# Kernel tuning notes

Hardware: AMD Instinct MI355X
Metric: run time of the kernel (lower is better)

The kernel has to match this reference:

```python
import jax, jax.numpy as jnp
import numpy as np
from jax.scipy.linalg import expm

B, D, CUT, LAYERS = 256, 4, 10, 4
K = D * (D - 1) // 2            # beamsplitter pairs per interferometer
P = 4 * K + 6 * D               # params per CVQNN layer (=48 for D=4)


def _ops(c):
    a = jnp.diag(jnp.sqrt(jnp.arange(1, c, dtype=jnp.float32)), k=1).astype(jnp.complex64)
    return a, a.T, jnp.arange(c, dtype=jnp.float32)


def _apply_single(state, U, m):
    t = jnp.tensordot(state, U, axes=((m + 1,), (1,)))
    return jnp.moveaxis(t, -1, m + 1)


def _apply_two(state, U4, i, j):
    t = jnp.tensordot(state, U4, axes=((i + 1, j + 1), (2, 3)))
    return jnp.moveaxis(t, (-2, -1), (i + 1, j + 1))


def _mul_diag(state, diag, m, d, c):
    return state * diag.reshape((1,) * (m + 1) + (c,) + (1,) * (d - m - 1))


def _interferometer(state, th, ph, vph, a, adag, n, d, c):
    pairs = [(i, j) for i in range(d) for j in range(i + 1, d)]
    Aab = jnp.kron(adag, a)  # adag_i a_j on a mode pair

    def gen(t, p):
        tc = t.astype(jnp.complex64)
        pc = p.astype(jnp.complex64)
        return tc * (jnp.exp(1j * pc) * Aab - jnp.exp(-1j * pc) * Aab.conj().T)

    U = jax.vmap(expm)(jax.vmap(gen)(th, ph)).reshape(len(pairs), c, c, c, c)
    for k, (i, j) in enumerate(pairs):
        state = _apply_two(state, U[k], i, j)
    nc = n.astype(jnp.complex64)
    for m in range(d):
        state = _mul_diag(state, jnp.exp(1j * vph[m].astype(jnp.complex64) * nc), m, d, c)
    return state


def _layer(state, w, a, adag, n, d, c):
    k = d * (d - 1) // 2
    o = 0
    th1 = w[o:o + k]; o += k
    ph1 = w[o:o + k]; o += k
    vp1 = w[o:o + d]; o += d
    rsq = w[o:o + d]; o += d
    th2 = w[o:o + k]; o += k
    ph2 = w[o:o + k]; o += k
    vp2 = w[o:o + d]; o += d
    rd = w[o:o + d]; o += d
    phd = w[o:o + d]; o += d
    kap = w[o:o + d]

    state = _interferometer(state, th1, ph1, vp1, a, adag, n, d, c)
    # per-mode squeezing S(r) = exp(r/2 (a^2 - adag^2))
    Ss = jax.vmap(lambda r: expm(0.5 * r.astype(jnp.complex64) * (a @ a - adag @ adag)))(rsq)
    for m in range(d):
        state = _apply_single(state, Ss[m], m)
    state = _interferometer(state, th2, ph2, vp2, a, adag, n, d, c)
    # per-mode displacement D(alpha)
    alpha = rd.astype(jnp.complex64) * jnp.exp(1j * phd.astype(jnp.complex64))
    Ds = jax.vmap(lambda al: expm(al * adag - jnp.conj(al) * a))(alpha)
    for m in range(d):
        state = _apply_single(state, Ds[m], m)
    # per-mode Kerr: diag(exp(i kappa n^2))
    nc = n.astype(jnp.complex64)
    for m in range(d):
        state = _mul_diag(state, jnp.exp(1j * kap[m].astype(jnp.complex64) * nc * nc), m, d, c)
    return state


def _forward(inputs, weights):
    d, c = D, CUT
    a, adag, n = _ops(c)
    # BatchPrepare: per mode |psi> = Displacement(r, 0) Squeezing(0.5, pi/2) |0>
    z = 0.5j  # r=0.5, phi=pi/2
    S0 = expm(0.5 * (jnp.conj(z) * (a @ a) - z * (adag @ adag)))
    psi0 = S0[:, 0]  # S |0>
    Dm = jax.vmap(lambda r: expm(r.astype(jnp.complex64) * (adag - a)))(inputs.reshape(-1))
    psi = (Dm @ psi0).reshape(inputs.shape[0], d, c)  # [B, d, c]
    # tensor product over modes -> [B, c, ..., c]
    state = psi[:, 0]
    for m in range(1, d):
        state = jnp.einsum('b...,bc->b...c', state, psi[:, m])
    for l in range(LAYERS):
        state = _layer(state, weights[l], a, adag, n, d, c)
    probs = jnp.abs(state) ** 2  # no normalization (Config(normalize=False))
    outs = [jnp.sum(_mul_diag(probs, n, m, d, c), axis=tuple(range(1, d + 1))) for m in range(d)]
    return jnp.stack(outs, axis=1)  # [B, modes] mean photon numbers


def setup_inputs() -> dict:
    key = jax.random.key(0)
    k1, k2 = jax.random.split(key)
    inputs = 0.3 * jax.random.normal(k1, (B, D), dtype=jnp.float32)
    cvqnn_weights = 0.1 * jax.random.normal(k2, (LAYERS, P), dtype=jnp.float32)
    return {"inputs": inputs, "cvqnn_weights": cvqnn_weights, "batch_size": B}


def reference(inputs, cvqnn_weights, batch_size):
    assert inputs.shape[0] == batch_size
    return _forward(inputs, cvqnn_weights)
```

## Files before the change

### kernel.cpp

```cpp
#include <hip/hip_runtime.h>
#include <hip/hip_bf16.h>

#define CUT 10
#define NB 256
#define NLAYERS 4
#define WSTRIDE 48

#define R_DM 0
#define R_SQ 1024
#define R_DS 1040
#define R_BS 1056
#define NRSLOTS 1968

#define F0 1110
#define F1 111
#define F2 11
#define F3 1
#define ST_PHYS 11100

#define LUT_A  0
#define LUT_B  60
#define LUT_C  120
#define LUT_I  234
#define LUT_S  253
#define LUT_IS 259
#define LUT_K  260
#define LUT_N  300

typedef __hip_bfloat16 bf16;

__device__ __forceinline__ float readv(const void* p, int i, int isf32) {
  if (isf32) return ((const float*)p)[i];
  return __bfloat162float(((const bf16*)p)[i]);
}

__device__ __forceinline__ void rmacL(float2& a, float2 mm, float2 v) {
  asm("v_pk_fma_f32 %0, %1, %2, %0 op_sel:[0,0,0] op_sel_hi:[0,1,1]"
      : "+v"(a) : "v"(mm), "v"(v));
}
__device__ __forceinline__ void rmacH(float2& a, float2 mm, float2 v) {
  asm("v_pk_fma_f32 %0, %1, %2, %0 op_sel:[1,0,0] op_sel_hi:[1,1,1]"
      : "+v"(a) : "v"(mm), "v"(v));
}

__device__ __forceinline__ float2 cmul(float2 u, float2 v) {
  float2 d;
  asm("v_pk_mul_f32 %0, %1, %2 op_sel:[0,0] op_sel_hi:[0,1]\n\t"
      "v_pk_fma_f32 %0, %1, %2, %0 op_sel:[1,1,0] op_sel_hi:[1,0,1] neg_lo:[1,0,0]"
      : "=&v"(d) : "v"(u), "v"(v));
  return d;
}

__device__ __forceinline__ float2 loF(const float4& q) { return make_float2(q.x, q.y); }
__device__ __forceinline__ float2 hiF(const float4& q) { return make_float2(q.z, q.w); }

__device__ const signed char g_perm[16][3] = {
  {18,-1,-1},{19,-1,-1},{16, 0,-1},{17, 1,-1},{20,36,-1},{21,37,-1},
  {14, 6,34},{15, 7,35},{22,30,-1},{23,31,-1},{12, 8, 4},{13, 9, 5},
  {24,28,32},{25,29,33},{10,26, 2},{11,27, 3}
};

__global__ void sniff_dtype(const void* p, int n_elems, int* flag) {
  __shared__ float red[256];
  const unsigned short* h = (const unsigned short*)p;
  int t = threadIdx.x;
  float mx = 0.f;
  for (int i = t; i < n_elems; i += 256) {
    unsigned short u = h[i];
    bf16 bv = *(const bf16*)&u;
    float v = fabsf(__bfloat162float(bv));
    if (!(v < 1e30f)) v = 1e30f;
    mx = fmaxf(mx, v);
  }
  red[t] = mx;
  __syncthreads();
  for (int off = 128; off > 0; off >>= 1) {
    if (t < off) red[t] = fmaxf(red[t], red[t + off]);
    __syncthreads();
  }
  if (t == 0) *flag = (red[0] > 1000.f) ? 1 : 0;
}

__global__ void build_gens(float* rslots, float2* s0, const void* inp,
                           const void* w, const int* flag) {
  int s = blockIdx.x;
  int t = threadIdx.x;
  if (t >= 100) return;
// ... 149 lines not shown
    if (t < 100) R[t] = acc;
    __syncthreads();
  }
  if (t < 100) G[t] = R[t];
}

__device__ __forceinline__ void gate_fs(const void* w, int isf32, int l, int half,
                                        int g, float& f0, float& f1, float& f3,
                                        float& fdc) {
  int po = l*WSTRIDE + (half ? 26 : 6);
  int vo = l*WSTRIDE + (half ? 32 : 12);
  f0 = 0.f; f1 = 0.f; f3 = 0.f;
  switch (g) {
    case 0: fdc = readv(w, po+0, isf32) - readv(w, po+1, isf32); break;
    case 1: fdc = readv(w, po+1, isf32) - readv(w, po+2, isf32); break;
    case 2: f0 = -readv(w, po+3, isf32); fdc = readv(w, po+2, isf32); break;
    case 3: fdc = readv(w, po+3, isf32) - readv(w, po+4, isf32); break;
    case 4: f1 = -readv(w, po+5, isf32); fdc = readv(w, po+4, isf32); break;
    default: {
      float vp0 = readv(w, vo+0, isf32), vp1 = readv(w, vo+1, isf32);
      float vp2 = readv(w, vo+2, isf32), vp3 = readv(w, vo+3, isf32);
      if (half) {
        vp0 -= readv(w, l*WSTRIDE+40+0, isf32);
        vp1 -= readv(w, l*WSTRIDE+40+1, isf32);
        vp2 -= readv(w, l*WSTRIDE+40+2, isf32);
        vp3 -= readv(w, l*WSTRIDE+40+3, isf32);
      }
      f0 = vp0; f1 = vp1; f3 = vp3;
      fdc = vp2 + readv(w, po+5, isf32) - vp3;
    }
  }
}

#define LOADQ(DST, P) do { _Pragma("unroll") \
  for (int q_ = 0; q_ < 5; ++q_) DST[q_] = Uq[(P)*5 + q_]; } while (0)

#define BS_PAIR(UA, R0)                                                        \
  {                                                                            \
    float2 a0 = make_float2(0.f,0.f), a1 = make_float2(0.f,0.f);               \
    _Pragma("unroll")                                                          \
    for (int j = 0; j < 5; ++j) if (2*j < sd) {                                \
      const float2 m0 = (j==0)?loF(UA[0]):(j==1)?hiF(UA[0]):(j==2)?loF(UA[1])  \
                        :(j==3)?hiF(UA[1]):loF(UA[2]);                         \
      const float2 m1 = (j==0)?hiF(UA[2]):(j==1)?loF(UA[3]):(j==2)?hiF(UA[3])  \
                        :(j==3)?loF(UA[4]):hiF(UA[4]);                         \
      rmacL(a0, m0, v[2*j]); rmacH(a0, m0, v[2*j+1]);                          \
      rmacL(a1, m1, v[2*j]); rmacH(a1, m1, v[2*j+1]);                          \
    }                                                                          \
    a0 = cmul(a0, rot); rot = cmul(rot, step);                                 \
    base[(R0)*se] = a0;                                                        \
    if ((R0) + 1 < sd) {                                                       \
      a1 = cmul(a1, rot); rot = cmul(rot, step);                               \
      base[((R0)+1)*se] = a1;                                                  \
    }                                                                          \
  }

template<int sI, int sJ, int sA, int sB, bool INROT>
__device__ __forceinline__ void bs_chunk(
    float2* st, const float* __restrict__ U, int sd,
    int hi10, int lo10, int lo, int N,
    float2 rot, float2 step, float2 ir, float2 istep)
{
  constexpr int se = sI - sJ;
  float2* base = st + hi10*sA + lo10*sB + lo*sI + (N - lo)*sJ;
  float2 v[10];
#pragma unroll
  for (int k = 0; k < 10; ++k) {
    if (k < sd) {
      float2 tv = base[k*se];
      if (INROT) { tv = cmul(tv, ir); ir = cmul(ir, istep); }
      v[k] = tv;
    } else {
      v[k] = make_float2(0.f, 0.f);
    }
  }
  const float4* Uq = (const float4*)U;
  float4 ua[5], ub[5];
  LOADQ(ua, 0);
#pragma unroll
  for (int p = 0; p < 5; p += 2) {
    if (2*p < sd) {
      if (2*p + 2 < sd) LOADQ(ub, p + 1);
      BS_PAIR(ua, 2*p);
    }
    if (2*p + 2 < sd) {
      if (2*p + 4 < sd) LOADQ(ua, p + 2);
      BS_PAIR(ub, 2*p + 2);
    }
  }
}

template<int sI, int sJ, int sA, int sB, bool INROT>
__device__ __forceinline__ void bs_gate(
    float2* st, const float* __restrict__ Ub, const float2* __restrict__ lut,
    int g, int lane, int ch0, int ch1, int ch2)
{
  const float2 step  = lut[LUT_S + g];
  const float2 istep = INROT ? lut[LUT_IS] : make_float2(1.f, 0.f);
#pragma unroll
  for (int r = 0; r < 3; ++r) {
    const int c = (r == 0) ? ch0 : (r == 1) ? ch1 : ch2;
    if (c >= 0) {
      int N = c >> 1;
      int spec = ((c & 1) << 6) + lane;
      if (spec < 100) {
        int lo = max(0, N - 9);
        const int sd = __builtin_amdgcn_readfirstlane(min(9, N) - lo + 1);
        int hi10 = spec / 10, lo10 = spec % 10;
        float2 rot = cmul(cmul(lut[LUT_A + g*10 + hi10], lut[LUT_B + g*10 + lo10]),
                          lut[LUT_C + g*19 + N]);
        float2 ir = INROT ? lut[LUT_I + N] : make_float2(1.f, 0.f);
        bs_chunk<sI,sJ,sA,sB,INROT>(st, Ub + N*100, sd, hi10, lo10, lo, N,
                                    rot, step, ir, istep);
      }
    }
  }
}

#define SM_PAIR(UA, R0)                                                        \
  {                                                                            \
    float2 a0 = make_float2(0.f,0.f), a1 = make_float2(0.f,0.f);               \
    _Pragma("unroll")                                                          \
    for (int j = 0; j < 5; ++j) {                                              \
      const float2 m0 = (j==0)?loF(UA[0]):(j==1)?hiF(UA[0]):(j==2)?loF(UA[1])  \
                        :(j==3)?hiF(UA[1]):loF(UA[2]);                         \
      const float2 m1 = (j==0)?hiF(UA[2]):(j==1)?loF(UA[3]):(j==2)?hiF(UA[3])  \
                        :(j==3)?loF(UA[4]):hiF(UA[4]);                         \
      rmacL(a0, m0, v[2*j]); rmacH(a0, m0, v[2*j+1]);                          \
      rmacL(a1, m1, v[2*j]); rmacH(a1, m1, v[2*j+1]);                          \
    }                                                                          \
    if (KERR) {                                                                \
      a0 = cmul(a0, cmul(kb, lut[LUT_K + 30 + (R0)]));                         \
      a1 = cmul(a1, cmul(kb, lut[LUT_K + 30 + (R0) + 1]));                     \
    }                                                                          \
    base[(R0)*sM] = a0;                                                        \
    base[((R0)+1)*sM] = a1;                                                    \
  }

template<int sM, int pA, int pB, int pC, bool KERR>
__device__ __forceinline__ void sm_gate(
    float2* st, const float* __restrict__ U, const float2* __restrict__ lut,
    bool smv, int q0, int q1, int q2)
{
  if (!smv) return;
  float2* base = st + q0*pA + q1*pB + q2*pC;
  float2 kb = make_float2(1.f, 0.f);
  if (KERR) kb = cmul(cmul(lut[LUT_K + q0], lut[LUT_K + 10 + q1]),
                      lut[LUT_K + 20 + q2]);
  float2 v[10];
#pragma unroll
  for (int k = 0; k < 10; ++k) v[k] = base[k*sM];
  const float4* Uq = (const float4*)U;
  float4 ua[5], ub[5];
  LOADQ(ua, 0);
#pragma unroll
  for (int p = 0; p < 5; p += 2) {
    {
      if (p < 4) LOADQ(ub, p + 1);
      SM_PAIR(ua, 2*p);
    }
    if (p + 1 < 5) {
      if (p + 2 < 5) LOADQ(ua, p + 2);
      SM_PAIR(ub, 2*(p + 1));
    }
  }
}

__global__ __launch_bounds__(1024, 4)
void fused_circuit(
    const float* __restrict__ rslots, const float2* __restrict__ s0,
    const void* __restrict__ w, const int* __restrict__ flag,
    float* __restrict__ out)
{
  __shared__ float2 st[ST_PHYS];
  __shared__ __align__(16) float smU[3200];
  __shared__ __align__(16) float bsU[2*1900];
  __shared__ float2 lut[LUT_N];
  __shared__ float2 psi[4][10];
  __shared__ float redw[64];
  const int b = blockIdx.x, t = threadIdx.x;
  const int wv = t >> 6, lane = t & 63;
  const int isf32 = *flag;

  const int ch0 = g_perm[wv][0], ch1 = g_perm[wv][1], ch2 = g_perm[wv][2];
  const bool smv = (t < 1000);
  const int q0 = t / 100, q1 = (t / 10) % 10, q2 = t % 10;

  if (t < 40) {
    int m = t / 10, r = t % 10;
    const float* Dmr = rslots + (size_t)(R_DM + b*4 + m) * 100;
    float2 acc = make_float2(0.f, 0.f);
    for (int c = 0; c < 10; ++c) {
      float a = Dmr[r*10 + c];
      float2 vv = s0[c * 10];
      acc.x += a * vv.x;
      acc.y += a * vv.y;
    }
    psi[m][r] = acc;
  }
  for (int i = t; i < 800; i += 1024)
    ((float4*)smU)[i] = ((const float4*)(rslots + (size_t)R_SQ * 100))[i];
  for (int i = t; i < 475; i += 1024)
    ((float4*)bsU)[i] = ((const float4*)(rslots + (size_t)R_BS * 100))[i];
  __syncthreads();
  for (int e = t; e < 10000; e += 1024) {
    int ph = e + e/10 + e/100;
    float2 z  = psi[0][e/1000];
    float2 w1 = psi[1][(e/100)%10];
    float2 r1 = make_float2(z.x*w1.x - z.y*w1.y, z.x*w1.y + z.y*w1.x);
    float2 w2 = psi[2][(e/10)%10];
    float2 r2 = make_float2(r1.x*w2.x - r1.y*w2.y, r1.x*w2.y + r1.y*w2.x);
    float2 w3 = psi[3][e%10];
    st[ph] = make_float2(r2.x*w3.x - r2.y*w3.y, r2.x*w3.y + r2.y*w3.x);
  }
  __syncthreads();

  float4 pf;
  auto pf_load = [&](int next) {
    if (next < 48 && t < 475)
      pf = ((const float4*)(rslots + (size_t)(R_BS + next*19) * 100))[t];
  };
  auto pf_store = [&](int next) {
    if (next < 48 && t < 475)
      ((float4*)(bsU + (next & 1) * 1900))[t] = pf;
  };

#pragma unroll 1
  for (int l = 0; l < NLAYERS; ++l) {
#pragma unroll 1
    for (int half = 0; half < 2; ++half) {
      const int g6 = l*12 + half*6;

      {
        const int po = l*WSTRIDE + (half ? 26 : 6);
        if (t < LUT_N) {
          float ang = 0.f;
          if (t < 120) {
            int isB = (t >= 60);
            int id = isB ? t - 60 : t;
            int g = id / 10, q = id % 10;
            float f0, f1, f3, fd;
            gate_fs(w, isf32, l, half, g, f0, f1, f3, fd);
            ang = (isB ? f1 : f0) * (float)q;
          } else if (t < 234) {
            int id = t - 120; int g = id / 19, N = id % 19;
            float f0, f1, f3, fd;
            gate_fs(w, isf32, l, half, g, f0, f1, f3, fd);
            int lo = max(0, N - 9);
            ang = f3 * (float)N + fd * (float)lo;
          } else if (t < 253) {
            int N = t - 234; int lo = max(0, N - 9);
            ang = -readv(w, po + 0, isf32) * (float)lo;
          } else if (t < 259) {
            int g = t - 253;
            float f0, f1, f3, fd;
            gate_fs(w, isf32, l, half, g, f0, f1, f3, fd);
            ang = fd;
          } else if (t == 259) {
            ang = -readv(w, po + 0, isf32);
          } else {
            int id = t - 260; int m = id / 10, q = id % 10;
            if (half) {
              float kap = readv(w, l*WSTRIDE + 44 + m, isf32);
              float pd  = readv(w, l*WSTRIDE + 40 + m, isf32);
              ang = kap * (float)(q*q) + pd * (float)q;
            }
          }
          float sn, cs; sincosf(ang, &sn, &cs);
          lut[t] = make_float2(cs, sn);
        }
        __syncthreads();
      }

      pf_load(g6+1);
      bs_gate<F0,F1,F2,F3,true >(st, bsU+((g6+0)&1)*1900, lut, 0, lane, ch0,ch1,ch2);
      pf_store(g6+1);
      __syncthreads();
      pf_load(g6+2);
      bs_gate<F0,F2,F1,F3,false>(st, bsU+((g6+1)&1)*1900, lut, 1, lane, ch0,ch1,ch2);
      pf_store(g6+2);
      __syncthreads();
      pf_load(g6+3);
      bs_gate<F0,F3,F1,F2,false>(st, bsU+((g6+2)&1)*1900, lut, 2, lane, ch0,ch1,ch2);
      pf_store(g6+3);
      __syncthreads();
      pf_load(g6+4);
      bs_gate<F1,F2,F0,F3,false>(st, bsU+((g6+3)&1)*1900, lut, 3, lane, ch0,ch1,ch2);
      pf_store(g6+4);
      __syncthreads();
      pf_load(g6+5);
      bs_gate<F1,F3,F0,F2,false>(st, bsU+((g6+4)&1)*1900, lut, 4, lane, ch0,ch1,ch2);
      pf_store(g6+5);
      __syncthreads();
      pf_load(g6+6);
      bs_gate<F2,F3,F0,F1,false>(st, bsU+((g6+5)&1)*1900, lut, 5, lane, ch0,ch1,ch2);
      pf_store(g6+6);
      __syncthreads();

      const int ub_ = (half == 0) ? (l*4) : (16 + l*4);
      sm_gate<F0,F1,F2,F3,false>(st, smU+(ub_+0)*100, lut, smv, q0,q1,q2);
      __syncthreads();
      sm_gate<F1,F0,F2,F3,false>(st, smU+(ub_+1)*100, lut, smv, q0,q1,q2);
      __syncthreads();
      sm_gate<F2,F0,F1,F3,false>(st, smU+(ub_+2)*100, lut, smv, q0,q1,q2);
      __syncthreads();
      if (half)
        sm_gate<F3,F0,F1,F2,true >(st, smU+(ub_+3)*100, lut, smv, q0,q1,q2);
      else
        sm_gate<F3,F0,F1,F2,false>(st, smU+(ub_+3)*100, lut, smv, q0,q1,q2);
      __syncthreads();
    }
  }

  float a0 = 0.f, a1 = 0.f, a2 = 0.f, a3 = 0.f;
  for (int e = t; e < 10000; e += 1024) {
    int ph = e + e/10 + e/100;
    float2 z = st[ph];
    float pz = z.x*z.x + z.y*z.y;
    a0 += pz * (float)(e/1000);
    a1 += pz * (float)((e/100)%10);
    a2 += pz * (float)((e/10)%10);
    a3 += pz * (float)(e%10);
  }
  for (int off2 = 32; off2 > 0; off2 >>= 1) {
    a0 += __shfl_down(a0, off2, 64);
    a1 += __shfl_down(a1, off2, 64);
    a2 += __shfl_down(a2, off2, 64);
    a3 += __shfl_down(a3, off2, 64);
  }
  if (lane == 0) {
    redw[wv*4+0] = a0; redw[wv*4+1] = a1;
    redw[wv*4+2] = a2; redw[wv*4+3] = a3;
  }
  __syncthreads();
  if (t < 4) {
    float s = 0.f;
    for (int ww = 0; ww < 16; ++ww) s += redw[ww*4 + t];
    out[b*4 + t] = s;
  }
}

extern "C" void kernel_launch(void* const* d_in, const int* in_sizes, int n_in,
                              void* d_out, int out_size, void* d_ws, size_t ws_size,
// ... 15 lines not shown
```

Before: 349.4 us.

## Double-buffer phase LUT and interleave beamsplitter chunk loads across chunks

The per-half phase LUT is now double-buffered and built for the next half during the last squeezing gate, which removes one barrier and the serialized LUT-build phase per half. The beamsplitter gate is restructured so two chunks' state vectors are loaded up front and the third chunk's load overlaps the previous chunk's compute. Rotation recurrences now use doubled steps, giving two independent chains. The per-wave channel indices are made scalar with readfirstlane. This raises register pressure because two 10-element vectors are live at once.

After: 424.6 us. +21.5%, slower.

```diff
diff --git a/kernel.cpp b/kernel.cpp
--- a/kernel.cpp
+++ b/kernel.cpp
@@ -25,7 +25,10 @@
 #define LUT_S  253
 #define LUT_IS 259
 #define LUT_K  260
-#define LUT_N  300
+#define LUT_S2 300
+#define LUT_IS2 306
+#define LUT_N  307
+#define LUT_PAD 320
 
 typedef __hip_bfloat16 bf16;
 
@@ -50,9 +53,6 @@
       : "=&v"(d) : "v"(u), "v"(v));
   return d;
 }
-
-__device__ __forceinline__ float2 loF(const float4& q) { return make_float2(q.x, q.y); }
-__device__ __forceinline__ float2 hiF(const float4& q) { return make_float2(q.z, q.w); }
 
 __device__ const signed char g_perm[16][3] = {
   {18,-1,-1},{19,-1,-1},{16, 0,-1},{17, 1,-1},{20,36,-1},{21,37,-1},
@@ -268,138 +268,209 @@
   }
 }
 
-#define LOADQ(DST, P) do { _Pragma("unroll") \
-  for (int q_ = 0; q_ < 5; ++q_) DST[q_] = Uq[(P)*5 + q_]; } while (0)
-
-#define BS_PAIR(UA, R0)                                                        \
-  {                                                                            \
-    float2 a0 = make_float2(0.f,0.f), a1 = make_float2(0.f,0.f);               \
-    _Pragma("unroll")                                                          \
-    for (int j = 0; j < 5; ++j) if (2*j < sd) {                                \
-      const float2 m0 = (j==0)?loF(UA[0]):(j==1)?hiF(UA[0]):(j==2)?loF(UA[1])  \
-                        :(j==3)?hiF(UA[1]):loF(UA[2]);                         \
-      const float2 m1 = (j==0)?hiF(UA[2]):(j==1)?loF(UA[3]):(j==2)?hiF(UA[3])  \
-                        :(j==3)?loF(UA[4]):hiF(UA[4]);                         \
-      rmacL(a0, m0, v[2*j]); rmacH(a0, m0, v[2*j+1]);                          \
-      rmacL(a1, m1, v[2*j]); rmacH(a1, m1, v[2*j+1]);                          \
-    }                                                                          \
-    a0 = cmul(a0, rot); rot = cmul(rot, step);                                 \
-    base[(R0)*se] = a0;                                                        \
-    if ((R0) + 1 < sd) {                                                       \
-      a1 = cmul(a1, rot); rot = cmul(rot, step);                               \
-      base[((R0)+1)*se] = a1;                                                  \
-    }                                                                          \
+__device__ __forceinline__ void build_lut(float2* lb, const void* w, int isf32,
+                                          int l, int half, int t) {
+  const int po = l*WSTRIDE + (half ? 26 : 6);
+  if (t < LUT_N) {
+    float ang = 0.f;
+    if (t < 120) {
+      int isB = (t >= 60);
+      int id = isB ? t - 60 : t;
+      int g = id / 10, q = id % 10;
+      float f0, f1, f3, fd;
+      gate_fs(w, isf32, l, half, g, f0, f1, f3, fd);
+      ang = (isB ? f1 : f0) * (float)q;
+    } else if (t < 234) {
+      int id = t - 120; int g = id / 19, N = id % 19;
+      float f0, f1, f3, fd;
+      gate_fs(w, isf32, l, half, g, f0, f1, f3, fd);
+      int lo = max(0, N - 9);
+      ang = f3 * (float)N + fd * (float)lo;
+    } else if (t < 253) {
+      int N = t - 234; int lo = max(0, N - 9);
+      ang = -readv(w, po + 0, isf32) * (float)lo;
+    } else if (t < 259) {
+      int g = t - 253;
+      float f0, f1, f3, fd;
+      gate_fs(w, isf32, l, half, g, f0, f1, f3, fd);
+      ang = fd;
+    } else if (t == 259) {
+      ang = -readv(w, po + 0, isf32);
+    } else if (t < 300) {
+      int id = t - 260; int m = id / 10, q = id % 10;
+      if (half) {
+        float kap = readv(w, l*WSTRIDE + 44 + m, isf32);
+        float pd  = readv(w, l*WSTRIDE + 40 + m, isf32);
+        ang = kap * (float)(q*q) + pd * (float)q;
+      }
+    } else if (t < 306) {
+      int g = t - 300;
+      float f0, f1, f3, fd;
+      gate_fs(w, isf32, l, half, g, f0, f1, f3, fd);
+      ang = 2.f * fd;
+    } else {
+      ang = -2.f * readv(w, po + 0, isf32);
+    }
+    float sn, cs; sincosf(ang, &sn, &cs);
+    lb[t] = make_float2(cs, sn);
+  }
+}
+
+#define BS_SETUP(IDX, C)                                                     \
+  int N##IDX = 0, sd##IDX = 0, hiA##IDX = 0, loA##IDX = 0;                   \
+  bool ok##IDX = false; float2* b##IDX = st;                                 \
+  if ((C) >= 0) {                                                            \
+    N##IDX = (C) >> 1;                                                       \
+    int spec_ = (((C) & 1) << 6) + lane;                                     \
+    int lo_ = max(0, N##IDX - 9);                                            \
+    sd##IDX = __builtin_amdgcn_readfirstlane(min(9, N##IDX) - lo_ + 1);      \
+    ok##IDX = (spec_ < 100);                                                 \
+    int spc_ = ok##IDX ? spec_ : 0;                                          \
+    hiA##IDX = spc_ / 10; loA##IDX = spc_ % 10;                              \
+    b##IDX = st + hiA##IDX*sA + loA##IDX*sB + lo_*sI + (N##IDX - lo_)*sJ;    \
+  }
+
+#define BS_LOAD(VV, IDX)                                                     \
+  { _Pragma("unroll")                                                        \
+    for (int k = 0; k < 10; ++k)                                             \
+      VV[k] = (k < sd##IDX) ? b##IDX[k*se] : make_float2(0.f, 0.f); }
+
+#define BS_INROT(VV, IDX)                                                    \
+  if (INROT && sd##IDX > 0) {                                                \
+    float2 ir0 = L[LUT_I + N##IDX];                                          \
+    float2 ir1 = cmul(ir0, istep1);                                          \
+    _Pragma("unroll")                                                        \
+    for (int k = 0; k < 10; k += 2) {                                        \
+      VV[k]   = cmul(VV[k],   ir0); ir0 = cmul(ir0, istep2);                 \
+      VV[k+1] = cmul(VV[k+1], ir1); ir1 = cmul(ir1, istep2);                 \
+    }                                                                        \
+  }
+
+#define BS_ROWPAIR(R0, VV)                                                   \
+  {                                                                          \
+    float2 a0 = make_float2(0.f,0.f), a1 = make_float2(0.f,0.f);             \
+    _Pragma("unroll")                                                        \
+    for (int j = 0; j < 5; ++j) if (2*j < sd_) {                             \
+      const float2 m0 = (j==0)?make_float2(qa0.x,qa0.y)                      \
+                       :(j==1)?make_float2(qa0.z,qa0.w)                      \
+                       :(j==2)?make_float2(qa1.x,qa1.y)                      \
+                       :(j==3)?make_float2(qa1.z,qa1.w)                      \
+                       :make_float2(qa2.x,qa2.y);                            \
+      const float2 m1 = (j==0)?make_float2(qa2.z,qa2.w)                      \
+                       :(j==1)?make_float2(qa3.x,qa3.y)                      \
+                       :(j==2)?make_float2(qa3.z,qa3.w)                      \
+                       :(j==3)?make_float2(qa4.x,qa4.y)                      \
+                       :make_float2(qa4.z,qa4.w);                            \
+      rmacL(a0, m0, VV[2*j]); rmacH(a0, m0, VV[2*j+1]);                      \
+      rmacL(a1, m1, VV[2*j]); rmacH(a1, m1, VV[2*j+1]);                      \
+    }                                                                        \
+    a0 = cmul(a0, rot0);                                                     \
+    if (ok_) bb[(R0)*se] = a0;                                               \
+    if ((R0) + 1 < sd_) {                                                    \
+      a1 = cmul(a1, rot1);                                                   \
+      if (ok_) bb[((R0)+1)*se] = a1;                                         \
+    }                                                                        \
+    rot0 = cmul(rot0, step2); rot1 = cmul(rot1, step2);                      \
+  }
+
+#define BS_COMP(VV, IDX)                                                     \
+  if (sd##IDX > 0) {                                                         \
+    const int sd_ = sd##IDX; const bool ok_ = ok##IDX;                       \
+    float2* bb = b##IDX;                                                     \
+    const float4* Uq = (const float4*)(Ub + N##IDX*100);                     \
+    float2 rot0 = cmul(cmul(L[LUT_A + g*10 + hiA##IDX],                      \
+                            L[LUT_B + g*10 + loA##IDX]),                     \
+                       L[LUT_C + g*19 + N##IDX]);                            \
+    float2 rot1 = cmul(rot0, step1);                                         \
+    float4 qa0,qa1,qa2,qa3,qa4;                                              \
+    qa0=Uq[0]; qa1=Uq[1]; qa2=Uq[2]; qa3=Uq[3]; qa4=Uq[4];                   \
+    BS_ROWPAIR(0, VV)                                                        \
+    if (sd_ > 2) { qa0=Uq[5]; qa1=Uq[6]; qa2=Uq[7]; qa3=Uq[8]; qa4=Uq[9];    \
+      BS_ROWPAIR(2, VV) }                                                    \
+    if (sd_ > 4) { qa0=Uq[10];qa1=Uq[11];qa2=Uq[12];qa3=Uq[13];qa4=Uq[14];   \
+      BS_ROWPAIR(4, VV) }                                                    \
+    if (sd_ > 6) { qa0=Uq[15];qa1=Uq[16];qa2=Uq[17];qa3=Uq[18];qa4=Uq[19];   \
+      BS_ROWPAIR(6, VV) }                                                    \
+    if (sd_ > 8) { qa0=Uq[20];qa1=Uq[21];qa2=Uq[22];qa3=Uq[23];qa4=Uq[24];   \
+      BS_ROWPAIR(8, VV) }                                                    \
   }
 
 template<int sI, int sJ, int sA, int sB, bool INROT>
-__device__ __forceinline__ void bs_chunk(
-    float2* st, const float* __restrict__ U, int sd,
-    int hi10, int lo10, int lo, int N,
-    float2 rot, float2 step, float2 ir, float2 istep)
+__device__ __forceinline__ void bs_gate(
+    float2* st, const float* __restrict__ Ub, const float2* __restrict__ L,
+    int g, int lane, int ch0, int ch1, int ch2)
 {
   constexpr int se = sI - sJ;
-  float2* base = st + hi10*sA + lo10*sB + lo*sI + (N - lo)*sJ;
-  float2 v[10];
-#pragma unroll
-  for (int k = 0; k < 10; ++k) {
-    if (k < sd) {
-      float2 tv = base[k*se];
-      if (INROT) { tv = cmul(tv, ir); ir = cmul(ir, istep); }
-      v[k] = tv;
-    } else {
-      v[k] = make_float2(0.f, 0.f);
-    }
-  }
-  const float4* Uq = (const float4*)U;
-  float4 ua[5], ub[5];
-  LOADQ(ua, 0);
-#pragma unroll
-  for (int p = 0; p < 5; p += 2) {
-    if (2*p < sd) {
-      if (2*p + 2 < sd) LOADQ(ub, p + 1);
-      BS_PAIR(ua, 2*p);
-    }
-    if (2*p + 2 < sd) {
-      if (2*p + 4 < sd) LOADQ(ua, p + 2);
-      BS_PAIR(ub, 2*p + 2);
-    }
-  }
-}
-
-template<int sI, int sJ, int sA, int sB, bool INROT>
-__device__ __forceinline__ void bs_gate(
-    float2* st, const float* __restrict__ Ub, const float2* __restrict__ lut,
-    int g, int lane, int ch0, int ch1, int ch2)
-{
-  const float2 step  = lut[LUT_S + g];
-  const float2 istep = INROT ? lut[LUT_IS] : make_float2(1.f, 0.f);
-#pragma unroll
-  for (int r = 0; r < 3; ++r) {
-    const int c = (r == 0) ? ch0 : (r == 1) ? ch1 : ch2;
-    if (c >= 0) {
-      int N = c >> 1;
-      int spec = ((c & 1) << 6) + lane;
-      if (spec < 100) {
-        int lo = max(0, N - 9);
-        const int sd = __builtin_amdgcn_readfirstlane(min(9, N) - lo + 1);
-        int hi10 = spec / 10, lo10 = spec % 10;
-        float2 rot = cmul(cmul(lut[LUT_A + g*10 + hi10], lut[LUT_B + g*10 + lo10]),
-                          lut[LUT_C + g*19 + N]);
-        float2 ir = INROT ? lut[LUT_I + N] : make_float2(1.f, 0.f);
-        bs_chunk<sI,sJ,sA,sB,INROT>(st, Ub + N*100, sd, hi10, lo10, lo, N,
-                                    rot, step, ir, istep);
-      }
-    }
-  }
-}
-
-#define SM_PAIR(UA, R0)                                                        \
-  {                                                                            \
-    float2 a0 = make_float2(0.f,0.f), a1 = make_float2(0.f,0.f);               \
-    _Pragma("unroll")                                                          \
-    for (int j = 0; j < 5; ++j) {                                              \
-      const float2 m0 = (j==0)?loF(UA[0]):(j==1)?hiF(UA[0]):(j==2)?loF(UA[1])  \
-                        :(j==3)?hiF(UA[1]):loF(UA[2]);                         \
-      const float2 m1 = (j==0)?hiF(UA[2]):(j==1)?loF(UA[3]):(j==2)?hiF(UA[3])  \
-                        :(j==3)?loF(UA[4]):hiF(UA[4]);                         \
-      rmacL(a0, m0, v[2*j]); rmacH(a0, m0, v[2*j+1]);                          \
-      rmacL(a1, m1, v[2*j]); rmacH(a1, m1, v[2*j+1]);                          \
-    }                                                                          \
-    if (KERR) {                                                                \
-      a0 = cmul(a0, cmul(kb, lut[LUT_K + 30 + (R0)]));                         \
-      a1 = cmul(a1, cmul(kb, lut[LUT_K + 30 + (R0) + 1]));                     \
-    }                                                                          \
-    base[(R0)*sM] = a0;                                                        \
-    base[((R0)+1)*sM] = a1;                                                    \
+  const float2 step1  = L[LUT_S + g];
+  const float2 step2  = L[LUT_S2 + g];
+  const float2 istep1 = L[LUT_IS];
+  const float2 istep2 = L[LUT_IS2];
+
+  float2 vA[10], vB[10];
+  BS_SETUP(0, ch0)
+  BS_SETUP(1, ch1)
+  BS_SETUP(2, ch2)
+  BS_LOAD(vA, 0)
+  BS_LOAD(vB, 1)
+  BS_INROT(vA, 0)
+  BS_COMP(vA, 0)
+  BS_LOAD(vA, 2)
+  BS_INROT(vB, 1)
+  BS_COMP(vB, 1)
+  BS_INROT(vA, 2)
+  BS_COMP(vA, 2)
+}
+
+#define SM_PAIR(R0)                                                          \
+  {                                                                          \
+    float2 a0 = make_float2(0.f,0.f), a1 = make_float2(0.f,0.f);             \
+    _Pragma("unroll")                                                        \
+    for (int j = 0; j < 5; ++j) {                                            \
+      const float2 m0 = (j==0)?make_float2(qa0.x,qa0.y)                      \
+                       :(j==1)?make_float2(qa0.z,qa0.w)                      \
+                       :(j==2)?make_float2(qa1.x,qa1.y)                      \
+                       :(j==3)?make_float2(qa1.z,qa1.w)                      \
+                       :make_float2(qa2.x,qa2.y);                            \
+      const float2 m1 = (j==0)?make_float2(qa2.z,qa2.w)                      \
+                       :(j==1)?make_float2(qa3.x,qa3.y)                      \
+                       :(j==2)?make_float2(qa3.z,qa3.w)                      \
+                       :(j==3)?make_float2(qa4.x,qa4.y)                      \
+                       :make_float2(qa4.z,qa4.w);                            \
+      rmacL(a0, m0, v[2*j]); rmacH(a0, m0, v[2*j+1]);                        \
+      rmacL(a1, m1, v[2*j]); rmacH(a1, m1, v[2*j+1]);                        \
+    }                                                                        \
+    if (KERR) {                                                              \
+      a0 = cmul(a0, cmul(kb, L[LUT_K + 30 + (R0)]));                         \
+      a1 = cmul(a1, cmul(kb, L[LUT_K + 30 + (R0) + 1]));                     \
+    }                                                                        \
+    base[(R0)*sM]   = a0;                                                    \
+    base[((R0)+1)*sM] = a1;                                                  \
   }
 
 template<int sM, int pA, int pB, int pC, bool KERR>
 __device__ __forceinline__ void sm_gate(
-    float2* st, const float* __restrict__ U, const float2* __restrict__ lut,
+    float2* st, const float* __restrict__ U, const float2* __restrict__ L,
     bool smv, int q0, int q1, int q2)
 {
   if (!smv) return;
   float2* base = st + q0*pA + q1*pB + q2*pC;
   float2 kb = make_float2(1.f, 0.f);
-  if (KERR) kb = cmul(cmul(lut[LUT_K + q0], lut[LUT_K + 10 + q1]),
-                      lut[LUT_K + 20 + q2]);
+  if (KERR) kb = cmul(cmul(L[LUT_K + q0], L[LUT_K + 10 + q1]), L[LUT_K + 20 + q2]);
   float2 v[10];
 #pragma unroll
   for (int k = 0; k < 10; ++k) v[k] = base[k*sM];
   const float4* Uq = (const float4*)U;
-  float4 ua[5], ub[5];
-  LOADQ(ua, 0);
-#pragma unroll
-  for (int p = 0; p < 5; p += 2) {
-    {
-      if (p < 4) LOADQ(ub, p + 1);
-      SM_PAIR(ua, 2*p);
-    }
-    if (p + 1 < 5) {
-      if (p + 2 < 5) LOADQ(ua, p + 2);
-      SM_PAIR(ub, 2*(p + 1));
-    }
-  }
+  float4 qa0,qa1,qa2,qa3,qa4;
+  qa0=Uq[0]; qa1=Uq[1]; qa2=Uq[2]; qa3=Uq[3]; qa4=Uq[4];
+  SM_PAIR(0)
+  qa0=Uq[5]; qa1=Uq[6]; qa2=Uq[7]; qa3=Uq[8]; qa4=Uq[9];
+  SM_PAIR(2)
+  qa0=Uq[10];qa1=Uq[11];qa2=Uq[12];qa3=Uq[13];qa4=Uq[14];
+  SM_PAIR(4)
+  qa0=Uq[15];qa1=Uq[16];qa2=Uq[17];qa3=Uq[18];qa4=Uq[19];
+  SM_PAIR(6)
+  qa0=Uq[20];qa1=Uq[21];qa2=Uq[22];qa3=Uq[23];qa4=Uq[24];
+  SM_PAIR(8)
 }
 
 __global__ __launch_bounds__(1024, 4)
@@ -411,14 +482,17 @@
   __shared__ float2 st[ST_PHYS];
   __shared__ __align__(16) float smU[3200];
   __shared__ __align__(16) float bsU[2*1900];
-  __shared__ float2 lut[LUT_N];
+  __shared__ float2 lut[2][LUT_PAD];
   __shared__ float2 psi[4][10];
   __shared__ float redw[64];
   const int b = blockIdx.x, t = threadIdx.x;
   const int wv = t >> 6, lane = t & 63;
   const int isf32 = *flag;
 
-  const int ch0 = g_perm[wv][0], ch1 = g_perm[wv][1], ch2 = g_perm[wv][2];
+  const int wvu = __builtin_amdgcn_readfirstlane(wv);
+  const int ch0 = __builtin_amdgcn_readfirstlane((int)g_perm[wvu][0]);
+  const int ch1 = __builtin_amdgcn_readfirstlane((int)g_perm[wvu][1]);
+  const int ch2 = __builtin_amdgcn_readfirstlane((int)g_perm[wvu][2]);
   const bool smv = (t < 1000);
   const int q0 = t / 100, q1 = (t / 10) % 10, q2 = t % 10;
 
@@ -438,6 +512,7 @@
     ((float4*)smU)[i] = ((const float4*)(rslots + (size_t)R_SQ * 100))[i];
   for (int i = t; i < 475; i += 1024)
     ((float4*)bsU)[i] = ((const float4*)(rslots + (size_t)R_BS * 100))[i];
+  build_lut(lut[0], w, isf32, 0, 0, t);
   __syncthreads();
   for (int e = t; e < 10000; e += 1024) {
     int ph = e + e/10 + e/100;
@@ -461,90 +536,57 @@
       ((float4*)(bsU + (next & 1) * 1900))[t] = pf;
   };
 
+  int par = 0;
 #pragma unroll 1
   for (int l = 0; l < NLAYERS; ++l) {
 #pragma unroll 1
     for (int half = 0; half < 2; ++half) {
       const int g6 = l*12 + half*6;
-
-      {
-        const int po = l*WSTRIDE + (half ? 26 : 6);
-        if (t < LUT_N) {
-          float ang = 0.f;
-          if (t < 120) {
-            int isB = (t >= 60);
-            int id = isB ? t - 60 : t;
-            int g = id / 10, q = id % 10;
-            float f0, f1, f3, fd;
-            gate_fs(w, isf32, l, half, g, f0, f1, f3, fd);
-            ang = (isB ? f1 : f0) * (float)q;
-          } else if (t < 234) {
-            int id = t - 120; int g = id / 19, N = id % 19;
-            float f0, f1, f3, fd;
-            gate_fs(w, isf32, l, half, g, f0, f1, f3, fd);
-            int lo = max(0, N - 9);
-            ang = f3 * (float)N + fd * (float)lo;
-          } else if (t < 253) {
-            int N = t - 234; int lo = max(0, N - 9);
-            ang = -readv(w, po + 0, isf32) * (float)lo;
-          } else if (t < 259) {
-            int g = t - 253;
-            float f0, f1, f3, fd;
-            gate_fs(w, isf32, l, half, g, f0, f1, f3, fd);
-            ang = fd;
-          } else if (t == 259) {
-            ang = -readv(w, po + 0, isf32);
-          } else {
-            int id = t - 260; int m = id / 10, q = id % 10;
-            if (half) {
-              float kap = readv(w, l*WSTRIDE + 44 + m, isf32);
-              float pd  = readv(w, l*WSTRIDE + 40 + m, isf32);
-              ang = kap * (float)(q*q) + pd * (float)q;
-            }
-          }
-          float sn, cs; sincosf(ang, &sn, &cs);
-          lut[t] = make_float2(cs, sn);
-        }
-        __syncthreads();
+      const float2* L = lut[par];
+
+      pf_load(g6+1);
+      bs_gate<F0,F1,F2,F3,true >(st, bsU+((g6+0)&1)*1900, L, 0, lane, ch0,ch1,ch2);
+      pf_store(g6+1);
+      __syncthreads();
+      pf_load(g6+2);
+      bs_gate<F0,F2,F1,F3,false>(st, bsU+((g6+1)&1)*1900, L, 1, lane, ch0,ch1,ch2);
+      pf_store(g6+2);
+      __syncthreads();
+      pf_load(g6+3);
+      bs_gate<F0,F3,F1,F2,false>(st, bsU+((g6+2)&1)*1900, L, 2, lane, ch0,ch1,ch2);
+      pf_store(g6+3);
+      __syncthreads();
+      pf_load(g6+4);
+      bs_gate<F1,F2,F0,F3,false>(st, bsU+((g6+3)&1)*1900, L, 3, lane, ch0,ch1,ch2);
+      pf_store(g6+4);
+      __syncthreads();
+      pf_load(g6+5);
+      bs_gate<F1,F3,F0,F2,false>(st, bsU+((g6+4)&1)*1900, L, 4, lane, ch0,ch1,ch2);
+      pf_store(g6+5);
+      __syncthreads();
+      pf_load(g6+6);
+      bs_gate<F2,F3,F0,F1,false>(st, bsU+((g6+5)&1)*1900, L, 5, lane, ch0,ch1,ch2);
+      pf_store(g6+6);
+      __syncthreads();
+
+      const int ub_ = (half == 0) ? (l*4) : (16 + l*4);
+      sm_gate<F0,F1,F2,F3,false>(st, smU+(ub_+0)*100, L, smv, q0,q1,q2);
+      __syncthreads();
+      sm_gate<F1,F0,F2,F3,false>(st, smU+(ub_+1)*100, L, smv, q0,q1,q2);
+      __syncthreads();
+      sm_gate<F2,F0,F1,F3,false>(st, smU+(ub_+2)*100, L, smv, q0,q1,q2);
+      __syncthreads();
+      if (half)
+        sm_gate<F3,F0,F1,F2,true >(st, smU+(ub_+3)*100, L, smv, q0,q1,q2);
+      else
+        sm_gate<F3,F0,F1,F2,false>(st, smU+(ub_+3)*100, L, smv, q0,q1,q2);
+      if (!(l == NLAYERS-1 && half == 1)) {
+        int nl = (half == 1) ? l + 1 : l;
+        int nh = half ^ 1;
+        build_lut(lut[par ^ 1], w, isf32, nl, nh, t);
       }
-
-      pf_load(g6+1);
-      bs_gate<F0,F1,F2,F3,true >(st, bsU+((g6+0)&1)*1900, lut, 0, lane, ch0,ch1,ch2);
-      pf_store(g6+1);
-      __syncthreads();
-      pf_load(g6+2);
-      bs_gate<F0,F2,F1,F3,false>(st, bsU+((g6+1)&1)*1900, lut, 1, lane, ch0,ch1,ch2);
-      pf_store(g6+2);
-      __syncthreads();
-      pf_load(g6+3);
-      bs_gate<F0,F3,F1,F2,false>(st, bsU+((g6+2)&1)*1900, lut, 2, lane, ch0,ch1,ch2);
-      pf_store(g6+3);
-      __syncthreads();
-      pf_load(g6+4);
-      bs_gate<F1,F2,F0,F3,false>(st, bsU+((g6+3)&1)*1900, lut, 3, lane, ch0,ch1,ch2);
-      pf_store(g6+4);
-      __syncthreads();
-      pf_load(g6+5);
-      bs_gate<F1,F3,F0,F2,false>(st, bsU+((g6+4)&1)*1900, lut, 4, lane, ch0,ch1,ch2);
-      pf_store(g6+5);
-      __syncthreads();
-      pf_load(g6+6);
-      bs_gate<F2,F3,F0,F1,false>(st, bsU+((g6+5)&1)*1900, lut, 5, lane, ch0,ch1,ch2);
-      pf_store(g6+6);
-      __syncthreads();
-
-      const int ub_ = (half == 0) ? (l*4) : (16 + l*4);
-      sm_gate<F0,F1,F2,F3,false>(st, smU+(ub_+0)*100, lut, smv, q0,q1,q2);
-      __syncthreads();
-      sm_gate<F1,F0,F2,F3,false>(st, smU+(ub_+1)*100, lut, smv, q0,q1,q2);
-      __syncthreads();
-      sm_gate<F2,F0,F1,F3,false>(st, smU+(ub_+2)*100, lut, smv, q0,q1,q2);
-      __syncthreads();
-      if (half)
-        sm_gate<F3,F0,F1,F2,true >(st, smU+(ub_+3)*100, lut, smv, q0,q1,q2);
-      else
-        sm_gate<F3,F0,F1,F2,false>(st, smU+(ub_+3)*100, lut, smv, q0,q1,q2);
-      __syncthreads();
+      __syncthreads();
+      par ^= 1;
     }
   }
 
```

## Double-buffer phase LUT and build next stage's LUT during Kerr gate

Applied to the files above, without the earlier changes.

The per-half phase lookup table becomes double-buffered. The next half's table is built in the same barrier interval as the last squeezing/Kerr gate, which removes one __syncthreads and the serial LUT-build phase per half-layer. The beamsplitter phase recurrences are also split into two independent chains with doubled step factors, shortening the dependent complex-multiply chain. Wave-uniform gate-chunk indices are forced into scalar registers via readfirstlane. This costs extra LDS, a few more LUT entries, and slightly different rounding in the phase products.

Measured after the change: 405.5 us. 16.1% more time.

```diff
diff --git a/kernel.cpp b/kernel.cpp
--- a/kernel.cpp
+++ b/kernel.cpp
@@ -25,7 +25,10 @@
 #define LUT_S  253
 #define LUT_IS 259
 #define LUT_K  260
-#define LUT_N  300
+#define LUT_S2 300
+#define LUT_IS2 306
+#define LUT_N  307
+#define LUT_PAD 320
 
 typedef __hip_bfloat16 bf16;
 
@@ -50,9 +53,6 @@
       : "=&v"(d) : "v"(u), "v"(v));
   return d;
 }
-
-__device__ __forceinline__ float2 loF(const float4& q) { return make_float2(q.x, q.y); }
-__device__ __forceinline__ float2 hiF(const float4& q) { return make_float2(q.z, q.w); }
 
 __device__ const signed char g_perm[16][3] = {
   {18,-1,-1},{19,-1,-1},{16, 0,-1},{17, 1,-1},{20,36,-1},{21,37,-1},
@@ -268,71 +268,135 @@
   }
 }
 
-#define LOADQ(DST, P) do { _Pragma("unroll") \
-  for (int q_ = 0; q_ < 5; ++q_) DST[q_] = Uq[(P)*5 + q_]; } while (0)
+__device__ __forceinline__ void build_lut(float2* lb, const void* w, int isf32,
+                                          int l, int half, int t) {
+  const int po = l*WSTRIDE + (half ? 26 : 6);
+  if (t < LUT_N) {
+    float ang = 0.f;
+    if (t < 120) {
+      int isB = (t >= 60);
+      int id = isB ? t - 60 : t;
+      int g = id / 10, q = id % 10;
+      float f0, f1, f3, fd;
+      gate_fs(w, isf32, l, half, g, f0, f1, f3, fd);
+      ang = (isB ? f1 : f0) * (float)q;
+    } else if (t < 234) {
+      int id = t - 120; int g = id / 19, N = id % 19;
+      float f0, f1, f3, fd;
+      gate_fs(w, isf32, l, half, g, f0, f1, f3, fd);
+      int lo = max(0, N - 9);
+      ang = f3 * (float)N + fd * (float)lo;
+    } else if (t < 253) {
+      int N = t - 234; int lo = max(0, N - 9);
+      ang = -readv(w, po + 0, isf32) * (float)lo;
+    } else if (t < 259) {
+      int g = t - 253;
+      float f0, f1, f3, fd;
+      gate_fs(w, isf32, l, half, g, f0, f1, f3, fd);
+      ang = fd;
+    } else if (t == 259) {
+      ang = -readv(w, po + 0, isf32);
+    } else if (t < 300) {
+      int id = t - 260; int m = id / 10, q = id % 10;
+      if (half) {
+        float kap = readv(w, l*WSTRIDE + 44 + m, isf32);
+        float pd  = readv(w, l*WSTRIDE + 40 + m, isf32);
+        ang = kap * (float)(q*q) + pd * (float)q;
+      }
+    } else if (t < 306) {
+      int g = t - 300;
+      float f0, f1, f3, fd;
+      gate_fs(w, isf32, l, half, g, f0, f1, f3, fd);
+      ang = 2.f * fd;
+    } else {
+      ang = -2.f * readv(w, po + 0, isf32);
+    }
+    float sn, cs; sincosf(ang, &sn, &cs);
+    lb[t] = make_float2(cs, sn);
+  }
+}
 
 #define BS_PAIR(UA, R0)                                                        \
   {                                                                            \
     float2 a0 = make_float2(0.f,0.f), a1 = make_float2(0.f,0.f);               \
     _Pragma("unroll")                                                          \
     for (int j = 0; j < 5; ++j) if (2*j < sd) {                                \
-      const float2 m0 = (j==0)?loF(UA[0]):(j==1)?hiF(UA[0]):(j==2)?loF(UA[1])  \
-                        :(j==3)?hiF(UA[1]):loF(UA[2]);                         \
-      const float2 m1 = (j==0)?hiF(UA[2]):(j==1)?loF(UA[3]):(j==2)?hiF(UA[3])  \
-                        :(j==3)?loF(UA[4]):hiF(UA[4]);                         \
+      const float2 m0 = (j==0)?make_float2(UA[0].x,UA[0].y)                    \
+                       :(j==1)?make_float2(UA[0].z,UA[0].w)                    \
+                       :(j==2)?make_float2(UA[1].x,UA[1].y)                    \
+                       :(j==3)?make_float2(UA[1].z,UA[1].w)                    \
+                       :make_float2(UA[2].x,UA[2].y);                          \
+      const float2 m1 = (j==0)?make_float2(UA[2].z,UA[2].w)                    \
+                       :(j==1)?make_float2(UA[3].x,UA[3].y)                    \
+                       :(j==2)?make_float2(UA[3].z,UA[3].w)                    \
+                       :(j==3)?make_float2(UA[4].x,UA[4].y)                    \
+                       :make_float2(UA[4].z,UA[4].w);                          \
       rmacL(a0, m0, v[2*j]); rmacH(a0, m0, v[2*j+1]);                          \
       rmacL(a1, m1, v[2*j]); rmacH(a1, m1, v[2*j+1]);                          \
     }                                                                          \
-    a0 = cmul(a0, rot); rot = cmul(rot, step);                                 \
+    a0 = cmul(a0, rot0);                                                       \
     base[(R0)*se] = a0;                                                        \
     if ((R0) + 1 < sd) {                                                       \
-      a1 = cmul(a1, rot); rot = cmul(rot, step);                               \
+      a1 = cmul(a1, rot1);                                                     \
       base[((R0)+1)*se] = a1;                                                  \
     }                                                                          \
+    rot0 = cmul(rot0, step2); rot1 = cmul(rot1, step2);                        \
   }
 
 template<int sI, int sJ, int sA, int sB, bool INROT>
 __device__ __forceinline__ void bs_chunk(
     float2* st, const float* __restrict__ U, int sd,
     int hi10, int lo10, int lo, int N,
-    float2 rot, float2 step, float2 ir, float2 istep)
+    float2 rot0, float2 step1, float2 step2,
+    float2 ir0, float2 is1, float2 is2)
 {
   constexpr int se = sI - sJ;
   float2* base = st + hi10*sA + lo10*sB + lo*sI + (N - lo)*sJ;
   float2 v[10];
 #pragma unroll
-  for (int k = 0; k < 10; ++k) {
-    if (k < sd) {
-      float2 tv = base[k*se];
-      if (INROT) { tv = cmul(tv, ir); ir = cmul(ir, istep); }
-      v[k] = tv;
-    } else {
-      v[k] = make_float2(0.f, 0.f);
-    }
-  }
+  for (int k = 0; k < 10; ++k)
+    v[k] = (k < sd) ? base[k*se] : make_float2(0.f, 0.f);
+  if (INROT) {
+    float2 i0 = ir0, i1 = cmul(ir0, is1);
+#pragma unroll
+    for (int k = 0; k < 10; k += 2) {
+      v[k]   = cmul(v[k],   i0); i0 = cmul(i0, is2);
+      v[k+1] = cmul(v[k+1], i1); i1 = cmul(i1, is2);
+    }
+  }
+  float2 rot1 = cmul(rot0, step1);
   const float4* Uq = (const float4*)U;
   float4 ua[5], ub[5];
-  LOADQ(ua, 0);
+#pragma unroll
+  for (int q = 0; q < 5; ++q) ua[q] = Uq[q];
 #pragma unroll
   for (int p = 0; p < 5; p += 2) {
     if (2*p < sd) {
-      if (2*p + 2 < sd) LOADQ(ub, p + 1);
-      BS_PAIR(ua, 2*p);
+      if (2*p + 2 < sd) {
+#pragma unroll
+        for (int q = 0; q < 5; ++q) ub[q] = Uq[(p+1)*5 + q];
+      }
+      BS_PAIR(ua, 2*p)
     }
     if (2*p + 2 < sd) {
-      if (2*p + 4 < sd) LOADQ(ua, p + 2);
-      BS_PAIR(ub, 2*p + 2);
+      if (2*p + 4 < sd) {
+#pragma unroll
+        for (int q = 0; q < 5; ++q) ua[q] = Uq[(p+2)*5 + q];
+      }
+      BS_PAIR(ub, 2*p + 2)
     }
   }
 }
 
 template<int sI, int sJ, int sA, int sB, bool INROT>
 __device__ __forceinline__ void bs_gate(
-    float2* st, const float* __restrict__ Ub, const float2* __restrict__ lut,
+    float2* st, const float* __restrict__ Ub, const float2* __restrict__ L,
     int g, int lane, int ch0, int ch1, int ch2)
 {
-  const float2 step  = lut[LUT_S + g];
-  const float2 istep = INROT ? lut[LUT_IS] : make_float2(1.f, 0.f);
+  const float2 step1 = L[LUT_S + g];
+  const float2 step2 = L[LUT_S2 + g];
+  const float2 is1   = L[LUT_IS];
+  const float2 is2   = L[LUT_IS2];
 #pragma unroll
   for (int r = 0; r < 3; ++r) {
     const int c = (r == 0) ? ch0 : (r == 1) ? ch1 : ch2;
@@ -343,11 +407,11 @@
         int lo = max(0, N - 9);
         const int sd = __builtin_amdgcn_readfirstlane(min(9, N) - lo + 1);
         int hi10 = spec / 10, lo10 = spec % 10;
-        float2 rot = cmul(cmul(lut[LUT_A + g*10 + hi10], lut[LUT_B + g*10 + lo10]),
-                          lut[LUT_C + g*19 + N]);
-        float2 ir = INROT ? lut[LUT_I + N] : make_float2(1.f, 0.f);
+        float2 rot0 = cmul(cmul(L[LUT_A + g*10 + hi10], L[LUT_B + g*10 + lo10]),
+                           L[LUT_C + g*19 + N]);
+        float2 ir0 = INROT ? L[LUT_I + N] : make_float2(1.f, 0.f);
         bs_chunk<sI,sJ,sA,sB,INROT>(st, Ub + N*100, sd, hi10, lo10, lo, N,
-                                    rot, step, ir, istep);
+                                    rot0, step1, step2, ir0, is1, is2);
       }
     }
   }
@@ -358,46 +422,58 @@
     float2 a0 = make_float2(0.f,0.f), a1 = make_float2(0.f,0.f);               \
     _Pragma("unroll")                                                          \
     for (int j = 0; j < 5; ++j) {                                              \
-      const float2 m0 = (j==0)?loF(UA[0]):(j==1)?hiF(UA[0]):(j==2)?loF(UA[1])  \
-                        :(j==3)?hiF(UA[1]):loF(UA[2]);                         \
-      const float2 m1 = (j==0)?hiF(UA[2]):(j==1)?loF(UA[3]):(j==2)?hiF(UA[3])  \
-                        :(j==3)?loF(UA[4]):hiF(UA[4]);                         \
+      const float2 m0 = (j==0)?make_float2(UA[0].x,UA[0].y)                    \
+                       :(j==1)?make_float2(UA[0].z,UA[0].w)                    \
+                       :(j==2)?make_float2(UA[1].x,UA[1].y)                    \
+                       :(j==3)?make_float2(UA[1].z,UA[1].w)                    \
+                       :make_float2(UA[2].x,UA[2].y);                          \
+      const float2 m1 = (j==0)?make_float2(UA[2].z,UA[2].w)                    \
+                       :(j==1)?make_float2(UA[3].x,UA[3].y)                    \
+                       :(j==2)?make_float2(UA[3].z,UA[3].w)                    \
+                       :(j==3)?make_float2(UA[4].x,UA[4].y)                    \
+                       :make_float2(UA[4].z,UA[4].w);                          \
       rmacL(a0, m0, v[2*j]); rmacH(a0, m0, v[2*j+1]);                          \
       rmacL(a1, m1, v[2*j]); rmacH(a1, m1, v[2*j+1]);                          \
     }                                                                          \
     if (KERR) {                                                                \
-      a0 = cmul(a0, cmul(kb, lut[LUT_K + 30 + (R0)]));                         \
-      a1 = cmul(a1, cmul(kb, lut[LUT_K + 30 + (R0) + 1]));                     \
+      a0 = cmul(a0, cmul(kb, L[LUT_K + 30 + (R0)]));                           \
+      a1 = cmul(a1, cmul(kb, L[LUT_K + 30 + (R0) + 1]));                       \
     }                                                                          \
-    base[(R0)*sM] = a0;                                                        \
+    base[(R0)*sM]   = a0;                                                      \
     base[((R0)+1)*sM] = a1;                                                    \
   }
 
 template<int sM, int pA, int pB, int pC, bool KERR>
 __device__ __forceinline__ void sm_gate(
-    float2* st, const float* __restrict__ U, const float2* __restrict__ lut,
+    float2* st, const float* __restrict__ U, const float2* __restrict__ L,
     bool smv, int q0, int q1, int q2)
 {
   if (!smv) return;
   float2* base = st + q0*pA + q1*pB + q2*pC;
   float2 kb = make_float2(1.f, 0.f);
-  if (KERR) kb = cmul(cmul(lut[LUT_K + q0], lut[LUT_K + 10 + q1]),
-                      lut[LUT_K + 20 + q2]);
+  if (KERR) kb = cmul(cmul(L[LUT_K + q0], L[LUT_K + 10 + q1]), L[LUT_K + 20 + q2]);
   float2 v[10];
 #pragma unroll
   for (int k = 0; k < 10; ++k) v[k] = base[k*sM];
   const float4* Uq = (const float4*)U;
   float4 ua[5], ub[5];
-  LOADQ(ua, 0);
+#pragma unroll
+  for (int q = 0; q < 5; ++q) ua[q] = Uq[q];
 #pragma unroll
   for (int p = 0; p < 5; p += 2) {
     {
-      if (p < 4) LOADQ(ub, p + 1);
-      SM_PAIR(ua, 2*p);
+      if (p < 4) {
+#pragma unroll
+        for (int q = 0; q < 5; ++q) ub[q] = Uq[(p+1)*5 + q];
+      }
+      SM_PAIR(ua, 2*p)
     }
     if (p + 1 < 5) {
-      if (p + 2 < 5) LOADQ(ua, p + 2);
-      SM_PAIR(ub, 2*(p + 1));
+      if (p + 2 < 5) {
+#pragma unroll
+        for (int q = 0; q < 5; ++q) ua[q] = Uq[(p+2)*5 + q];
+      }
+      SM_PAIR(ub, 2*(p+1))
     }
   }
 }
@@ -411,14 +487,17 @@
   __shared__ float2 st[ST_PHYS];
   __shared__ __align__(16) float smU[3200];
   __shared__ __align__(16) float bsU[2*1900];
-  __shared__ float2 lut[LUT_N];
+  __shared__ float2 lut[2][LUT_PAD];
   __shared__ float2 psi[4][10];
   __shared__ float redw[64];
   const int b = blockIdx.x, t = threadIdx.x;
   const int wv = t >> 6, lane = t & 63;
   const int isf32 = *flag;
 
-  const int ch0 = g_perm[wv][0], ch1 = g_perm[wv][1], ch2 = g_perm[wv][2];
+  const int wvu = __builtin_amdgcn_readfirstlane(wv);
+  const int ch0 = __builtin_amdgcn_readfirstlane((int)g_perm[wvu][0]);
+  const int ch1 = __builtin_amdgcn_readfirstlane((int)g_perm[wvu][1]);
+  const int ch2 = __builtin_amdgcn_readfirstlane((int)g_perm[wvu][2]);
   const bool smv = (t < 1000);
   const int q0 = t / 100, q1 = (t / 10) % 10, q2 = t % 10;
 
@@ -438,6 +517,7 @@
     ((float4*)smU)[i] = ((const float4*)(rslots + (size_t)R_SQ * 100))[i];
   for (int i = t; i < 475; i += 1024)
     ((float4*)bsU)[i] = ((const float4*)(rslots + (size_t)R_BS * 100))[i];
+  build_lut(lut[0], w, isf32, 0, 0, t);
   __syncthreads();
   for (int e = t; e < 10000; e += 1024) {
     int ph = e + e/10 + e/100;
@@ -461,90 +541,57 @@
       ((float4*)(bsU + (next & 1) * 1900))[t] = pf;
   };
 
+  int par = 0;
 #pragma unroll 1
   for (int l = 0; l < NLAYERS; ++l) {
 #pragma unroll 1
     for (int half = 0; half < 2; ++half) {
       const int g6 = l*12 + half*6;
-
-      {
-        const int po = l*WSTRIDE + (half ? 26 : 6);
-        if (t < LUT_N) {
-          float ang = 0.f;
-          if (t < 120) {
-            int isB = (t >= 60);
-            int id = isB ? t - 60 : t;
-            int g = id / 10, q = id % 10;
-            float f0, f1, f3, fd;
-            gate_fs(w, isf32, l, half, g, f0, f1, f3, fd);
-            ang = (isB ? f1 : f0) * (float)q;
-          } else if (t < 234) {
-            int id = t - 120; int g = id / 19, N = id % 19;
-            float f0, f1, f3, fd;
-            gate_fs(w, isf32, l, half, g, f0, f1, f3, fd);
-            int lo = max(0, N - 9);
-            ang = f3 * (float)N + fd * (float)lo;
-          } else if (t < 253) {
-            int N = t - 234; int lo = max(0, N - 9);
-            ang = -readv(w, po + 0, isf32) * (float)lo;
-          } else if (t < 259) {
-            int g = t - 253;
-            float f0, f1, f3, fd;
-            gate_fs(w, isf32, l, half, g, f0, f1, f3, fd);
-            ang = fd;
-          } else if (t == 259) {
-            ang = -readv(w, po + 0, isf32);
-          } else {
-            int id = t - 260; int m = id / 10, q = id % 10;
-            if (half) {
-              float kap = readv(w, l*WSTRIDE + 44 + m, isf32);
-              float pd  = readv(w, l*WSTRIDE + 40 + m, isf32);
-              ang = kap * (float)(q*q) + pd * (float)q;
-            }
-          }
-          float sn, cs; sincosf(ang, &sn, &cs);
-          lut[t] = make_float2(cs, sn);
-        }
-        __syncthreads();
-      }
+      const float2* L = lut[par];
 
       pf_load(g6+1);
-      bs_gate<F0,F1,F2,F3,true >(st, bsU+((g6+0)&1)*1900, lut, 0, lane, ch0,ch1,ch2);
+      bs_gate<F0,F1,F2,F3,true >(st, bsU+((g6+0)&1)*1900, L, 0, lane, ch0,ch1,ch2);
       pf_store(g6+1);
       __syncthreads();
       pf_load(g6+2);
-      bs_gate<F0,F2,F1,F3,false>(st, bsU+((g6+1)&1)*1900, lut, 1, lane, ch0,ch1,ch2);
+      bs_gate<F0,F2,F1,F3,false>(st, bsU+((g6+1)&1)*1900, L, 1, lane, ch0,ch1,ch2);
       pf_store(g6+2);
       __syncthreads();
       pf_load(g6+3);
-      bs_gate<F0,F3,F1,F2,false>(st, bsU+((g6+2)&1)*1900, lut, 2, lane, ch0,ch1,ch2);
+      bs_gate<F0,F3,F1,F2,false>(st, bsU+((g6+2)&1)*1900, L, 2, lane, ch0,ch1,ch2);
       pf_store(g6+3);
       __syncthreads();
       pf_load(g6+4);
-      bs_gate<F1,F2,F0,F3,false>(st, bsU+((g6+3)&1)*1900, lut, 3, lane, ch0,ch1,ch2);
+      bs_gate<F1,F2,F0,F3,false>(st, bsU+((g6+3)&1)*1900, L, 3, lane, ch0,ch1,ch2);
       pf_store(g6+4);
       __syncthreads();
       pf_load(g6+5);
-      bs_gate<F1,F3,F0,F2,false>(st, bsU+((g6+4)&1)*1900, lut, 4, lane, ch0,ch1,ch2);
+      bs_gate<F1,F3,F0,F2,false>(st, bsU+((g6+4)&1)*1900, L, 4, lane, ch0,ch1,ch2);
       pf_store(g6+5);
       __syncthreads();
       pf_load(g6+6);
-      bs_gate<F2,F3,F0,F1,false>(st, bsU+((g6+5)&1)*1900, lut, 5, lane, ch0,ch1,ch2);
+      bs_gate<F2,F3,F0,F1,false>(st, bsU+((g6+5)&1)*1900, L, 5, lane, ch0,ch1,ch2);
       pf_store(g6+6);
       __syncthreads();
 
       const int ub_ = (half == 0) ? (l*4) : (16 + l*4);
-      sm_gate<F0,F1,F2,F3,false>(st, smU+(ub_+0)*100, lut, smv, q0,q1,q2);
-      __syncthreads();
-      sm_gate<F1,F0,F2,F3,false>(st, smU+(ub_+1)*100, lut, smv, q0,q1,q2);
-      __syncthreads();
-      sm_gate<F2,F0,F1,F3,false>(st, smU+(ub_+2)*100, lut, smv, q0,q1,q2);
+      sm_gate<F0,F1,F2,F3,false>(st, smU+(ub_+0)*100, L, smv, q0,q1,q2);
+      __syncthreads();
+      sm_gate<F1,F0,F2,F3,false>(st, smU+(ub_+1)*100, L, smv, q0,q1,q2);
+      __syncthreads();
+      sm_gate<F2,F0,F1,F3,false>(st, smU+(ub_+2)*100, L, smv, q0,q1,q2);
       __syncthreads();
       if (half)
-        sm_gate<F3,F0,F1,F2,true >(st, smU+(ub_+3)*100, lut, smv, q0,q1,q2);
+        sm_gate<F3,F0,F1,F2,true >(st, smU+(ub_+3)*100, L, smv, q0,q1,q2);
       else
-        sm_gate<F3,F0,F1,F2,false>(st, smU+(ub_+3)*100, lut, smv, q0,q1,q2);
-      __syncthreads();
+        sm_gate<F3,F0,F1,F2,false>(st, smU+(ub_+3)*100, L, smv, q0,q1,q2);
+      if (!(l == NLAYERS-1 && half == 1)) {
+        int nl = (half == 1) ? l + 1 : l;
+        int nh = half ^ 1;
+        build_lut(lut[par ^ 1], w, isf32, nl, nh, t);
+      }
+      __syncthreads();
+      par ^= 1;
     }
   }
 
```
